# Kernel tuning notes

Hardware: AMD Instinct MI355X
Metric: run time of the kernel (lower is better)

## Reference

```python
import jax, jax.numpy as jnp
import numpy as np

N = 100000       # nodes
E = 3200000      # edges (avg degree 32)
IN_FEATS = 128
HIDDEN = 32
PROP_STEP = 8
USE_RELU = False  # args.relu default


def setup_inputs() -> dict:
    key = jax.random.key(0)
    k1, k2, k3, k4, k5 = jax.random.split(key, 5)
    in_feat = jax.random.normal(k1, (N, IN_FEATS), jnp.float32)
    src = jax.random.randint(k2, (E,), 0, N)
    dst = jax.random.randint(k3, (E,), 0, N)
    # Glorot-ish uniform init like DGL GraphConv weights
    s1 = float(np.sqrt(6.0 / (IN_FEATS + HIDDEN)))
    s2 = float(np.sqrt(6.0 / (HIDDEN + HIDDEN)))
    W1 = jax.random.uniform(k4, (IN_FEATS, HIDDEN), jnp.float32, -s1, s1)
    b1 = jnp.zeros((HIDDEN,), jnp.float32)
    W2 = jax.random.uniform(k5, (HIDDEN, HIDDEN), jnp.float32, -s2, s2)
    b2 = jnp.zeros((HIDDEN,), jnp.float32)
    return {"in_feat": in_feat, "W1": W1, "b1": b1, "W2": W2, "b2": b2,
            "src": src, "dst": dst}


def _graph_conv(x, W, b, src, dst, out_norm, in_norm, weight_first):
    # DGL GraphConv, norm='both':
    #   h = x * out_deg^{-1/2}; (optionally h @ W); SpMM aggregate src->dst;
    #   rst = agg * in_deg^{-1/2}; (optionally @ W); + bias
    h = x * out_norm[:, None]
    if weight_first:
        h = h @ W  # [N, out]
    agg = jax.ops.segment_sum(h[src], dst, num_segments=x.shape[0])
    rst = agg * in_norm[:, None]
    if not weight_first:
        rst = rst @ W
    return rst + b


def reference(in_feat, W1, b1, W2, b2, src, dst):
    n = in_feat.shape[0]
    ones = jnp.ones((src.shape[0],), in_feat.dtype)
    out_deg = jax.ops.segment_sum(ones, src, num_segments=n)
    in_deg = jax.ops.segment_sum(ones, dst, num_segments=n)
    out_norm = jax.lax.rsqrt(jnp.maximum(out_deg, 1.0))
    in_norm = jax.lax.rsqrt(jnp.maximum(in_deg, 1.0))
    # conv1: in_feats(128) > out_feats(32) -> weight applied before aggregation
    h = _graph_conv(in_feat, W1, b1, src, dst, out_norm, in_norm, weight_first=True)
    for _ in range(1, PROP_STEP):
        if USE_RELU:
            h = jax.nn.relu(h)
        h = _graph_conv(h, W2, b2, src, dst, out_norm, in_norm, weight_first=False)
    return h
```

## Files before the change

### kernel.cpp

```cpp
#include <hip/hip_runtime.h>
#include <hip/hip_bf16.h>

#define NNODES 100000
#define NEDGES 3200000
#define INF 128
#define HID 32
#define NB 392
#define BSHIFT 8
#define NPB 256
#define BATCH 8192
#define PART_BLOCKS ((NEDGES + BATCH - 1) / BATCH)
#define G1_ROWS 256
#define G1_KC 16
#define G1_XP 260

typedef unsigned short u16;

__device__ __forceinline__ float blo(unsigned x) { return __uint_as_float(x << 16); }
__device__ __forceinline__ float bhi(unsigned x) { return __uint_as_float(x & 0xffff0000u); }
__device__ __forceinline__ u16 f2b(float f) {
    __hip_bfloat16 h = __float2bfloat16(f);
    return *reinterpret_cast<u16*>(&h);
}

__global__ void k_cnt(const int* __restrict__ src, const int* __restrict__ dst,
                      int* __restrict__ bcnt_src, int* __restrict__ bcnt_dst) {
    __shared__ int hs[NB], hd[NB];
    int tid = threadIdx.x;
    for (int i = tid; i < NB; i += 1024) { hs[i] = 0; hd[i] = 0; }
    __syncthreads();
    int start = blockIdx.x * BATCH;
    int end = start + BATCH; if (end > NEDGES) end = NEDGES;
    for (int i = start + tid; i < end; i += 1024) {
        atomicAdd(&hs[src[i] >> BSHIFT], 1);
        atomicAdd(&hd[dst[i] >> BSHIFT], 1);
    }
    __syncthreads();
    for (int i = tid; i < NB; i += 1024) {
        if (hs[i]) atomicAdd(&bcnt_src[i], hs[i]);
        if (hd[i]) atomicAdd(&bcnt_dst[i], hd[i]);
    }
}

__global__ void k_bscan(const int* __restrict__ bcnt_src, const int* __restrict__ bcnt_dst,
                        int* __restrict__ bbase_src, int* __restrict__ bbase_dst,
                        int* __restrict__ gcur_src, int* __restrict__ gcur_dst) {
    __shared__ int s[512], t[512];
    int tid = threadIdx.x;
    int vs = (tid < NB) ? bcnt_src[tid] : 0;
    int vd = (tid < NB) ? bcnt_dst[tid] : 0;
    s[tid] = vs; t[tid] = vd;
    __syncthreads();
    for (int off = 1; off < 512; off <<= 1) {
        int a = (tid >= off) ? s[tid - off] : 0;
        int b = (tid >= off) ? t[tid - off] : 0;
        __syncthreads();
        s[tid] += a; t[tid] += b;
        __syncthreads();
    }
    if (tid < NB) {
        bbase_src[tid] = s[tid] - vs;  gcur_src[tid] = s[tid] - vs;
        bbase_dst[tid] = t[tid] - vd;  gcur_dst[tid] = t[tid] - vd;
    }
}

__global__ void k_bucket2(const int* __restrict__ src, const int* __restrict__ dst,
                          int* __restrict__ gcur_src, int* __restrict__ gcur_dst,
                          int2* __restrict__ pairbuf, int* __restrict__ srctmp) {
    __shared__ int2 stage2[BATCH];
    __shared__ int cnt[NB], excl[NB], gbase[NB];
    __shared__ int sc[512];
    int* stage1 = (int*)stage2;
    int tid = threadIdx.x;
    int start = blockIdx.x * BATCH;
    int end = start + BATCH; if (end > NEDGES) end = NEDGES;
    int cntE = end - start;

    int dd[8], sv[8], rk[8];

    for (int i = tid; i < NB; i += 1024) cnt[i] = 0;
    __syncthreads();
#pragma unroll
    for (int k = 0; k < 8; ++k) {
        int i = start + tid + k * 1024;
        dd[k] = -1;
        if (i < end) {
            dd[k] = dst[i]; sv[k] = src[i];
            rk[k] = atomicAdd(&cnt[dd[k] >> BSHIFT], 1);
        }
    }
    __syncthreads();
    if (tid < 512) sc[tid] = (tid < NB) ? cnt[tid] : 0;
    __syncthreads();
    for (int off = 1; off < 512; off <<= 1) {
        int v = (tid < 512 && tid >= off) ? sc[tid - off] : 0;
        __syncthreads();
        if (tid < 512) sc[tid] += v;
        __syncthreads();
    }
    if (tid < NB) {
        excl[tid] = sc[tid] - cnt[tid];
        int c = cnt[tid];
        gbase[tid] = c ? atomicAdd(&gcur_dst[tid], c) : 0;
    }
    __syncthreads();
#pragma unroll
    for (int k = 0; k < 8; ++k)
        if (dd[k] >= 0) {
            int2 e; e.x = dd[k]; e.y = sv[k];
            stage2[excl[dd[k] >> BSHIFT] + rk[k]] = e;
        }
    __syncthreads();
    for (int j = tid; j < cntE; j += 1024) {
        int2 e = stage2[j];
        int b = e.x >> BSHIFT;
        pairbuf[gbase[b] + (j - excl[b])] = e;
    }
    __syncthreads();

    for (int i = tid; i < NB; i += 1024) cnt[i] = 0;
    __syncthreads();
#pragma unroll
    for (int k = 0; k < 8; ++k)
        if (dd[k] >= 0)
            rk[k] = atomicAdd(&cnt[sv[k] >> BSHIFT], 1);
    __syncthreads();
    if (tid < 512) sc[tid] = (tid < NB) ? cnt[tid] : 0;
    __syncthreads();
    for (int off = 1; off < 512; off <<= 1) {
        int v = (tid < 512 && tid >= off) ? sc[tid - off] : 0;
        __syncthreads();
        if (tid < 512) sc[tid] += v;
        __syncthreads();
    }
    if (tid < NB) {
        excl[tid] = sc[tid] - cnt[tid];
        int c = cnt[tid];
        gbase[tid] = c ? atomicAdd(&gcur_src[tid], c) : 0;
    }
    __syncthreads();
#pragma unroll
    for (int k = 0; k < 8; ++k)
        if (dd[k] >= 0)
            stage1[excl[sv[k] >> BSHIFT] + rk[k]] = sv[k];
    __syncthreads();
    for (int j = tid; j < cntE; j += 1024) {
        int v = stage1[j];
        int b = v >> BSHIFT;
        srctmp[gbase[b] + (j - excl[b])] = v;
    }
}

__global__ void k_nodes(const int* __restrict__ srctmp, const int2* __restrict__ pairbuf,
                        const int* __restrict__ bbase_src, const int* __restrict__ bcnt_src,
                        const int* __restrict__ bbase_dst, const int* __restrict__ bcnt_dst,
                        float* __restrict__ out_norm, float* __restrict__ in_norm,
                        int* __restrict__ indeg, int* __restrict__ rowstart) {
    __shared__ int cnt[NPB];
    __shared__ int ss[NPB];
    int tid = threadIdx.x;
    int b = blockIdx.x;
    int srcphase = (b < NB);
    int bb = srcphase ? b : b - NB;
    int node0 = bb * NPB;
    cnt[tid] = 0;
    __syncthreads();
    if (srcphase) {
        int s0 = bbase_src[bb], n = bcnt_src[bb];
        for (int i = tid; i < n; i += 256)
            atomicAdd(&cnt[srctmp[s0 + i] - node0], 1);
        __syncthreads();
        int nn = node0 + tid;
        if (nn < NNODES) {
            int c = cnt[tid];
            out_norm[nn] = rsqrtf((float)(c > 1 ? c : 1));
        }
    } else {
        int d0 = bbase_dst[bb], n = bcnt_dst[bb];
        for (int i = tid; i < n; i += 256)
            atomicAdd(&cnt[pairbuf[d0 + i].x - node0], 1);
        __syncthreads();
        int c = cnt[tid];
        ss[tid] = c;
        __syncthreads();
        for (int off = 1; off < 256; off <<= 1) {
            int t = (tid >= off) ? ss[tid - off] : 0;
            __syncthreads();
            ss[tid] += t;
            __syncthreads();
        }
        int excl = ss[tid] - c;
        int nn = node0 + tid;
        if (nn < NNODES) {
            indeg[nn] = c;
            in_norm[nn] = rsqrtf((float)(c > 1 ? c : 1));
            rowstart[nn] = d0 + excl;
        }
    }
}

__global__ void k_place(const int2* __restrict__ pairbuf, const int* __restrict__ rowstart,
                        int* __restrict__ col) {
    __shared__ int cur[NPB];
    int tid = threadIdx.x;
    int bucket = blockIdx.x;
    int node0 = bucket * NPB;
    if (node0 >= NNODES) return;
    int n = node0 + tid;
    cur[tid] = (n < NNODES) ? rowstart[n] : 0;
    __syncthreads();
    int pstart = rowstart[node0];
    int pend   = (node0 + NPB >= NNODES) ? NEDGES : rowstart[node0 + NPB];
    for (int i = pstart + tid; i < pend; i += 256) {
        int2 e = pairbuf[i];
        int pos = atomicAdd(&cur[e.x - node0], 1);
        col[pos] = e.y;
    }
}

__global__ __launch_bounds__(256) void k_gemm1(const float* __restrict__ x,
                                               const float* __restrict__ W1,
                                               const float* __restrict__ out_norm,
                                               u16* __restrict__ t) {
    __shared__ float wlds[INF * HID];
    __shared__ float xT[G1_KC][G1_XP];
    int tid = threadIdx.x;
    int row0 = blockIdx.x * G1_ROWS;
    for (int i = tid; i < INF * HID; i += 256) wlds[i] = W1[i];

    int rg = tid >> 2;
    int cg = tid & 3;
    int sr = tid >> 2;
    int kq = tid & 3;

    float acc[4][8];
#pragma unroll
    for (int r = 0; r < 4; ++r)
#pragma unroll
        for (int c = 0; c < 8; ++c) acc[r][c] = 0.f;

    for (int kc = 0; kc < INF; kc += G1_KC) {
#pragma unroll
        for (int pass = 0; pass < 4; ++pass) {
            int r = pass * 64 + sr;
            int grow = row0 + r;
            float4 xv = make_float4(0.f, 0.f, 0.f, 0.f);
            if (grow < NNODES)
                xv = *(const float4*)(x + (size_t)grow * INF + kc + kq * 4);
            xT[kq * 4 + 0][r] = xv.x;
            xT[kq * 4 + 1][r] = xv.y;
            xT[kq * 4 + 2][r] = xv.z;
            xT[kq * 4 + 3][r] = xv.w;
        }
        __syncthreads();
#pragma unroll
        for (int kk = 0; kk < G1_KC; ++kk) {
            float4 xr = *(const float4*)&xT[kk][rg * 4];
            float4 wa = *(const float4*)&wlds[(kc + kk) * HID + cg * 8];
            float4 wb = *(const float4*)&wlds[(kc + kk) * HID + cg * 8 + 4];
            float xs[4] = {xr.x, xr.y, xr.z, xr.w};
#pragma unroll
            for (int r = 0; r < 4; ++r) {
                acc[r][0] = fmaf(xs[r], wa.x, acc[r][0]);
                acc[r][1] = fmaf(xs[r], wa.y, acc[r][1]);
                acc[r][2] = fmaf(xs[r], wa.z, acc[r][2]);
                acc[r][3] = fmaf(xs[r], wa.w, acc[r][3]);
                acc[r][4] = fmaf(xs[r], wb.x, acc[r][4]);
                acc[r][5] = fmaf(xs[r], wb.y, acc[r][5]);
                acc[r][6] = fmaf(xs[r], wb.z, acc[r][6]);
                acc[r][7] = fmaf(xs[r], wb.w, acc[r][7]);
            }
        }
        __syncthreads();
    }
#pragma unroll
    for (int r = 0; r < 4; ++r) {
        int row = row0 + rg * 4 + r;
        if (row < NNODES) {
            float on = out_norm[row];
            unsigned p0 = f2b(acc[r][0] * on) | ((unsigned)f2b(acc[r][1] * on) << 16);
            unsigned p1 = f2b(acc[r][2] * on) | ((unsigned)f2b(acc[r][3] * on) << 16);
            unsigned p2 = f2b(acc[r][4] * on) | ((unsigned)f2b(acc[r][5] * on) << 16);
            unsigned p3 = f2b(acc[r][6] * on) | ((unsigned)f2b(acc[r][7] * on) << 16);
            *(uint4*)(t + (size_t)row * HID + cg * 8) = make_uint4(p0, p1, p2, p3);
        }
    }
}

template<int APPLY_W, int FINAL>
__global__ void k_spmm(const u16* __restrict__ gin, const int* __restrict__ rowstart,
                       const int* __restrict__ indeg, const int* __restrict__ col,
                       const float* __restrict__ in_norm, const float* __restrict__ out_norm,
                       const float* __restrict__ W, const float* __restrict__ bias,
                       void* __restrict__ gout) {
    __shared__ float wlds[HID * HID];
    __shared__ float sh[8][HID];
    int tid = threadIdx.x, lane = tid & 31, group = tid >> 5;
    int g = lane >> 2, f = lane & 3;
    if (APPLY_W) {
        for (int i = tid; i < HID * HID; i += 256) wlds[i] = W[i];
        __syncthreads();
    }
    int n = blockIdx.x * 8 + group;
    int start = rowstart[n];
    int deg   = indeg[n];
    const uint4* gin16 = (const uint4*)gin;

    float a[8];
#pragma unroll
    for (int j = 0; j < 8; ++j) a[j] = 0.f;

    int base = 0;
    for (; base + 32 <= deg; base += 32) {
        int c = col[start + base + lane];
#pragma unroll
        for (int t = 0; t < 4; ++t) {
            int s = __shfl(c, t * 8 + g, 32);
            uint4 v = gin16[(size_t)s * 4 + f];
            a[0] += blo(v.x); a[1] += bhi(v.x);
            a[2] += blo(v.y); a[3] += bhi(v.y);
            a[4] += blo(v.z); a[5] += bhi(v.z);
            a[6] += blo(v.w); a[7] += bhi(v.w);
        }
    }
    if (base < deg) {
        int rem = deg - base;
        int c = (base + lane < deg) ? col[start + base + lane] : 0;
#pragma unroll
        for (int t = 0; t < 4; ++t) {
            if (t * 8 < rem) {
                int e = t * 8 + g;
                int s = __shfl(c, e, 32);
                uint4 v = gin16[(size_t)s * 4 + f];
                float m = (e < rem) ? 1.f : 0.f;
                a[0] = fmaf(m, blo(v.x), a[0]); a[1] = fmaf(m, bhi(v.x), a[1]);
                a[2] = fmaf(m, blo(v.y), a[2]); a[3] = fmaf(m, bhi(v.y), a[3]);
                a[4] = fmaf(m, blo(v.z), a[4]); a[5] = fmaf(m, bhi(v.z), a[5]);
                a[6] = fmaf(m, blo(v.w), a[6]); a[7] = fmaf(m, bhi(v.w), a[7]);
            }
        }
    }
#pragma unroll
    for (int j = 0; j < 8; ++j) {
        a[j] += __shfl_xor(a[j], 4, 32);
        a[j] += __shfl_xor(a[j], 8, 32);
        a[j] += __shfl_xor(a[j], 16, 32);
    }
    float inm = in_norm[n];
    if (g == 0) {
        float4 lo = make_float4(a[0] * inm, a[1] * inm, a[2] * inm, a[3] * inm);
        float4 hi = make_float4(a[4] * inm, a[5] * inm, a[6] * inm, a[7] * inm);
        *(float4*)&sh[group][f * 8]     = lo;
        *(float4*)&sh[group][f * 8 + 4] = hi;
    }
    float res;
    if (APPLY_W) {
        float o = bias[lane];
#pragma unroll
        for (int k = 0; k < HID; ++k)
            o += sh[group][k] * wlds[k * HID + lane];
        res = o;
    } else {
        res = sh[group][lane] + bias[lane];
    }
    if (FINAL) ((float*)gout)[(size_t)n * HID + lane] = res;
    else       ((u16*)gout)[(size_t)n * HID + lane] = f2b(res * out_norm[n]);
}

extern "C" void kernel_launch(void* const* d_in, const int* in_sizes, int n_in,
                              void* d_out, int out_size, void* d_ws, size_t ws_size,
                              hipStream_t stream) {
    const float* in_feat = (const float*)d_in[0];
    const float* W1      = (const float*)d_in[1];
    const float* b1      = (const float*)d_in[2];
    const float* W2      = (const float*)d_in[3];
    const float* b2      = (const float*)d_in[4];
    const int*   src     = (const int*)d_in[5];
    const int*   dst     = (const int*)d_in[6];
    float*       out     = (float*)d_out;

    const int N = NNODES, E = NEDGES;
    int* bcnt_src  = (int*)d_ws;
    int* bcnt_dst  = bcnt_src + 512;
    int* bbase_src = bcnt_dst + 512;
    int* bbase_dst = bbase_src + 512;
    int* gcur_src  = bbase_dst + 512;
    int* gcur_dst  = gcur_src + 512;
    int* indeg     = gcur_dst + 512;
    int* rowstart  = indeg + N;
    float* out_norm = (float*)(rowstart + N);
    float* in_norm  = out_norm + N;
    int*   col      = (int*)(in_norm + N);
    void*  bufreg   = (void*)(col + E);
    int2*  pairbuf  = (int2*)bufreg;
    int*   srctmp   = col;
    u16*   bufA16   = (u16*)bufreg;
    u16*   bufB16   = bufA16 + (size_t)N * HID;
    size_t need = ((size_t)3072 + 4 * N + E + (size_t)2 * N * HID) * 4;
    if (ws_size < need) return;

    hipMemsetAsync(bcnt_src, 0, 1024 * sizeof(int), stream);

    k_cnt    <<<PART_BLOCKS, 1024, 0, stream>>>(src, dst, bcnt_src, bcnt_dst);
    k_bscan  <<<1, 512, 0, stream>>>(bcnt_src, bcnt_dst, bbase_src, bbase_dst,
                                     gcur_src, gcur_dst);
    k_bucket2<<<PART_BLOCKS, 1024, 0, stream>>>(src, dst, gcur_src, gcur_dst,
                                                pairbuf, srctmp);
    k_nodes  <<<2 * NB, 256, 0, stream>>>(srctmp, pairbuf, bbase_src, bcnt_src,
                                          bbase_dst, bcnt_dst, out_norm, in_norm,
                                          indeg, rowstart);
    k_place  <<<NB, 256, 0, stream>>>(pairbuf, rowstart, col);

    k_gemm1<<<(N + G1_ROWS - 1) / G1_ROWS, 256, 0, stream>>>(in_feat, W1, out_norm, bufA16);

    k_spmm<0, 0><<<N / 8, 256, 0, stream>>>(bufA16, rowstart, indeg, col, in_norm,
                                            out_norm, W2, b1, bufB16);

    u16* cur = bufB16; u16* nxt = bufA16;
    for (int i = 0; i < 6; ++i) {
        k_spmm<1, 0><<<N / 8, 256, 0, stream>>>(cur, rowstart, indeg, col, in_norm,
                                                out_norm, W2, b2, nxt);
        u16* tmp = cur; cur = nxt; nxt = tmp;
    }
    k_spmm<1, 1><<<N / 8, 256, 0, stream>>>(cur, rowstart, indeg, col, in_norm,
                                            out_norm, W2, b2, out);
}
```

Baseline: 465.6 us.

## Split SpMM gather into two source-node halves for cache locality

New measurement: 626.5 us. 34.6% more time.

```diff
diff --git a/kernel.cpp b/kernel.cpp
--- a/kernel.cpp
+++ b/kernel.cpp
@@ -5,6 +5,7 @@
 #define NEDGES 3200000
 #define INF 128
 #define HID 32
+#define MID 50000
 #define NB 392
 #define BSHIFT 8
 #define NPB 256
@@ -15,12 +16,20 @@
 #define G1_XP 260
 
 typedef unsigned short u16;
+typedef float f4v __attribute__((ext_vector_type(4)));
 
 __device__ __forceinline__ float blo(unsigned x) { return __uint_as_float(x << 16); }
 __device__ __forceinline__ float bhi(unsigned x) { return __uint_as_float(x & 0xffff0000u); }
 __device__ __forceinline__ u16 f2b(float f) {
     __hip_bfloat16 h = __float2bfloat16(f);
     return *reinterpret_cast<u16*>(&h);
+}
+__device__ __forceinline__ void nt_store4(float* p, float a, float b, float c, float d) {
+    f4v v = {a, b, c, d};
+    __builtin_nontemporal_store(v, (f4v*)p);
+}
+__device__ __forceinline__ f4v nt_load4(const float* p) {
+    return __builtin_nontemporal_load((const f4v*)p);
 }
 
 __global__ void k_cnt(const int* __restrict__ src, const int* __restrict__ dst,
@@ -155,15 +164,17 @@
                         const int* __restrict__ bbase_src, const int* __restrict__ bcnt_src,
                         const int* __restrict__ bbase_dst, const int* __restrict__ bcnt_dst,
                         float* __restrict__ out_norm, float* __restrict__ in_norm,
-                        int* __restrict__ indeg, int* __restrict__ rowstart) {
+                        int* __restrict__ indeg, int* __restrict__ rowstart,
+                        int* __restrict__ rowmid) {
     __shared__ int cnt[NPB];
+    __shared__ int cntlow[NPB];
     __shared__ int ss[NPB];
     int tid = threadIdx.x;
     int b = blockIdx.x;
     int srcphase = (b < NB);
     int bb = srcphase ? b : b - NB;
     int node0 = bb * NPB;
-    cnt[tid] = 0;
+    cnt[tid] = 0; cntlow[tid] = 0;
     __syncthreads();
     if (srcphase) {
         int s0 = bbase_src[bb], n = bcnt_src[bb];
@@ -177,8 +188,11 @@
         }
     } else {
         int d0 = bbase_dst[bb], n = bcnt_dst[bb];
-        for (int i = tid; i < n; i += 256)
-            atomicAdd(&cnt[pairbuf[d0 + i].x - node0], 1);
+        for (int i = tid; i < n; i += 256) {
+            int2 e = pairbuf[d0 + i];
+            atomicAdd(&cnt[e.x - node0], 1);
+            if (e.y < MID) atomicAdd(&cntlow[e.x - node0], 1);
+        }
         __syncthreads();
         int c = cnt[tid];
         ss[tid] = c;
@@ -195,25 +209,28 @@
             indeg[nn] = c;
             in_norm[nn] = rsqrtf((float)(c > 1 ? c : 1));
             rowstart[nn] = d0 + excl;
+            rowmid[nn]   = d0 + excl + cntlow[tid];
         }
     }
 }
 
 __global__ void k_place(const int2* __restrict__ pairbuf, const int* __restrict__ rowstart,
-                        int* __restrict__ col) {
-    __shared__ int cur[NPB];
+                        const int* __restrict__ rowmid, int* __restrict__ col) {
+    __shared__ int curlo[NPB], curhi[NPB];
     int tid = threadIdx.x;
     int bucket = blockIdx.x;
     int node0 = bucket * NPB;
     if (node0 >= NNODES) return;
     int n = node0 + tid;
-    cur[tid] = (n < NNODES) ? rowstart[n] : 0;
+    curlo[tid] = (n < NNODES) ? rowstart[n] : 0;
+    curhi[tid] = (n < NNODES) ? rowmid[n] : 0;
     __syncthreads();
     int pstart = rowstart[node0];
     int pend   = (node0 + NPB >= NNODES) ? NEDGES : rowstart[node0 + NPB];
     for (int i = pstart + tid; i < pend; i += 256) {
         int2 e = pairbuf[i];
-        int pos = atomicAdd(&cur[e.x - node0], 1);
+        int j = e.x - node0;
+        int pos = (e.y < MID) ? atomicAdd(&curlo[j], 1) : atomicAdd(&curhi[j], 1);
         col[pos] = e.y;
     }
 }
@@ -287,23 +304,25 @@
     }
 }
 
-template<int APPLY_W, int FINAL>
+template<int RANGE, int APPLY_W, int FINAL>
 __global__ void k_spmm(const u16* __restrict__ gin, const int* __restrict__ rowstart,
-                       const int* __restrict__ indeg, const int* __restrict__ col,
-                       const float* __restrict__ in_norm, const float* __restrict__ out_norm,
-                       const float* __restrict__ W, const float* __restrict__ bias,
+                       const int* __restrict__ rowmid, const int* __restrict__ indeg,
+                       const int* __restrict__ col, const float* __restrict__ in_norm,
+                       const float* __restrict__ out_norm, const float* __restrict__ W,
+                       const float* __restrict__ bias, float* __restrict__ P,
                        void* __restrict__ gout) {
     __shared__ float wlds[HID * HID];
     __shared__ float sh[8][HID];
     int tid = threadIdx.x, lane = tid & 31, group = tid >> 5;
     int g = lane >> 2, f = lane & 3;
-    if (APPLY_W) {
+    if (RANGE == 1 && APPLY_W) {
         for (int i = tid; i < HID * HID; i += 256) wlds[i] = W[i];
         __syncthreads();
     }
     int n = blockIdx.x * 8 + group;
-    int start = rowstart[n];
-    int deg   = indeg[n];
+    int start, deg;
+    if (RANGE == 0) { start = rowstart[n]; deg = rowmid[n] - start; }
+    else            { start = rowmid[n];   deg = rowstart[n] + indeg[n] - start; }
     const uint4* gin16 = (const uint4*)gin;
 
     float a[8];
@@ -312,7 +331,7 @@
 
     int base = 0;
     for (; base + 32 <= deg; base += 32) {
-        int c = col[start + base + lane];
+        int c = __builtin_nontemporal_load(&col[start + base + lane]);
 #pragma unroll
         for (int t = 0; t < 4; ++t) {
             int s = __shfl(c, t * 8 + g, 32);
@@ -325,7 +344,8 @@
     }
     if (base < deg) {
         int rem = deg - base;
-        int c = (base + lane < deg) ? col[start + base + lane] : 0;
+        int c = (base + lane < deg)
+              ? __builtin_nontemporal_load(&col[start + base + lane]) : 0;
 #pragma unroll
         for (int t = 0; t < 4; ++t) {
             if (t * 8 < rem) {
@@ -346,10 +366,21 @@
         a[j] += __shfl_xor(a[j], 8, 32);
         a[j] += __shfl_xor(a[j], 16, 32);
     }
+    if (RANGE == 0) {
+        if (g == 0) {
+            nt_store4(&P[(size_t)n * HID + f * 8],     a[0], a[1], a[2], a[3]);
+            nt_store4(&P[(size_t)n * HID + f * 8 + 4], a[4], a[5], a[6], a[7]);
+        }
+        return;
+    }
     float inm = in_norm[n];
     if (g == 0) {
-        float4 lo = make_float4(a[0] * inm, a[1] * inm, a[2] * inm, a[3] * inm);
-        float4 hi = make_float4(a[4] * inm, a[5] * inm, a[6] * inm, a[7] * inm);
+        f4v plo = nt_load4(&P[(size_t)n * HID + f * 8]);
+        f4v phi = nt_load4(&P[(size_t)n * HID + f * 8 + 4]);
+        float4 lo = make_float4((a[0] + plo.x) * inm, (a[1] + plo.y) * inm,
+                                (a[2] + plo.z) * inm, (a[3] + plo.w) * inm);
+        float4 hi = make_float4((a[4] + phi.x) * inm, (a[5] + phi.y) * inm,
+                                (a[6] + phi.z) * inm, (a[7] + phi.w) * inm);
         *(float4*)&sh[group][f * 8]     = lo;
         *(float4*)&sh[group][f * 8 + 4] = hi;
     }
@@ -388,7 +419,8 @@
     int* gcur_dst  = gcur_src + 512;
     int* indeg     = gcur_dst + 512;
     int* rowstart  = indeg + N;
-    float* out_norm = (float*)(rowstart + N);
+    int* rowmid    = rowstart + N;
+    float* out_norm = (float*)(rowmid + N);
     float* in_norm  = out_norm + N;
     int*   col      = (int*)(in_norm + N);
     void*  bufreg   = (void*)(col + E);
@@ -396,7 +428,8 @@
     int*   srctmp   = col;
     u16*   bufA16   = (u16*)bufreg;
     u16*   bufB16   = bufA16 + (size_t)N * HID;
-    size_t need = ((size_t)3072 + 4 * N + E + (size_t)2 * N * HID) * 4;
+    float* Pf32     = (float*)(bufA16 + (size_t)2 * N * HID);
+    size_t need = ((size_t)3072 + 5 * N + E + (size_t)2 * N * HID) * 4;
     if (ws_size < need) return;
 
     hipMemsetAsync(bcnt_src, 0, 1024 * sizeof(int), stream);
@@ -408,20 +441,27 @@
                                                 pairbuf, srctmp);
     k_nodes  <<<2 * NB, 256, 0, stream>>>(srctmp, pairbuf, bbase_src, bcnt_src,
                                           bbase_dst, bcnt_dst, out_norm, in_norm,
-                                          indeg, rowstart);
-    k_place  <<<NB, 256, 0, stream>>>(pairbuf, rowstart, col);
+                                          indeg, rowstart, rowmid);
+    k_place  <<<NB, 256, 0, stream>>>(pairbuf, rowstart, rowmid, col);
 
     k_gemm1<<<(N + G1_ROWS - 1) / G1_ROWS, 256, 0, stream>>>(in_feat, W1, out_norm, bufA16);
 
-    k_spmm<0, 0><<<N / 8, 256, 0, stream>>>(bufA16, rowstart, indeg, col, in_norm,
-                                            out_norm, W2, b1, bufB16);
+    const int G = N / 8;
+    k_spmm<0, 0, 0><<<G, 256, 0, stream>>>(bufA16, rowstart, rowmid, indeg, col,
+                                           in_norm, out_norm, W2, b1, Pf32, bufB16);
+    k_spmm<1, 0, 0><<<G, 256, 0, stream>>>(bufA16, rowstart, rowmid, indeg, col,
+                                           in_norm, out_norm, W2, b1, Pf32, bufB16);
 
     u16* cur = bufB16; u16* nxt = bufA16;
     for (int i = 0; i < 6; ++i) {
-        k_spmm<1, 0><<<N / 8, 256, 0, stream>>>(cur, rowstart, indeg, col, in_norm,
-                                                out_norm, W2, b2, nxt);
+        k_spmm<0, 1, 0><<<G, 256, 0, stream>>>(cur, rowstart, rowmid, indeg, col,
+                                               in_norm, out_norm, W2, b2, Pf32, nxt);
+        k_spmm<1, 1, 0><<<G, 256, 0, stream>>>(cur, rowstart, rowmid, indeg, col,
+                                               in_norm, out_norm, W2, b2, Pf32, nxt);
         u16* tmp = cur; cur = nxt; nxt = tmp;
     }
-    k_spmm<1, 1><<<N / 8, 256, 0, stream>>>(cur, rowstart, indeg, col, in_norm,
-                                            out_norm, W2, b2, out);
-}
+    k_spmm<0, 1, 1><<<G, 256, 0, stream>>>(cur, rowstart, rowmid, indeg, col,
+                                           in_norm, out_norm, W2, b2, Pf32, out);
+    k_spmm<1, 1, 1><<<G, 256, 0, stream>>>(cur, rowstart, rowmid, indeg, col,
+                                           in_norm, out_norm, W2, b2, Pf32, out);
+}
```
